# Optimization experiments

Hardware: AMD Instinct MI355X
Metric: run time of the kernel (lower is better)

## Reference

```python
import jax, jax.numpy as jnp
import numpy as np

V, E, H, D = 32000, 512, 512, 3          # vocab, embed_dim, hidden_dim, max_depth
PD = max(H // 4, 16)                      # policy depth-embed dim = 128
DEPTH_EMBED_SCALE = 0.01
SIB_SCALE = 1.0 / np.sqrt(H)              # sibling_scale default 1/sqrt(hidden_dim)
GREEDY_THRESHOLD = 0.5
PROB_MIN, PROB_MAX = 1e-7, 1.0 - 1e-7


def _ln(x, g, b, eps=1e-5):
    m = x.mean(-1, keepdims=True)
    v = jnp.var(x, axis=-1, keepdims=True)
    return (x - m) * jax.lax.rsqrt(v + eps) * g + b


def setup_inputs() -> dict:
    key = jax.random.key(0)
    ks = jax.random.split(key, 12)
    def n(k, shape, s=0.02):
        return jax.random.normal(k, shape, jnp.float32) * s
    return {
        "token_ids": jax.random.randint(ks[0], (4096,), 0, V),
        "emb": n(ks[1], (V, E)),                      # embedding table
        "proj_w": n(ks[2], (H, E), 0.04), "proj_b": jnp.zeros(H, jnp.float32),
        "cf_w": n(ks[3], (2 * H, H), 0.04), "cf_b": jnp.zeros(2 * H, jnp.float32),
        "in_g": jnp.ones(H, jnp.float32), "in_b": jnp.zeros(H, jnp.float32),   # policy input LayerNorm
        "pde": n(ks[4], (D + 1, PD), 0.01),           # policy depth embedding
        "f1w": n(ks[5], (H // 2, H + PD), 0.04), "f1b": jnp.zeros(H // 2, jnp.float32),
        "n1g": jnp.ones(H // 2, jnp.float32), "n1b": jnp.zeros(H // 2, jnp.float32),
        "f2w": n(ks[6], (H // 4, H // 2), 0.06), "f2b": jnp.zeros(H // 4, jnp.float32),
        "n2g": jnp.ones(H // 4, jnp.float32), "n2b": jnp.zeros(H // 4, jnp.float32),
        "pow_w": n(ks[7], (1, H // 4), 0.01), "pow_b": jnp.zeros(1, jnp.float32),
        "sib": n(ks[8], (2, H)),                      # sibling embeddings (left/right)
        "dep": n(ks[9], (D + 1, H), 0.01),            # tree depth embeddings
        "out_w": n(ks[10], (V, H), 0.04), "out_b": jnp.zeros(V, jnp.float32),
    }


def _forward(token_ids, emb, proj_w, proj_b, cf_w, cf_b, in_g, in_b, pde,
             f1w, f1b, n1g, n1b, f2w, f2b, n2g, n2b, pow_w, pow_b,
             sib, dep, out_w, out_b):
    # h0: project token embeddings to hidden space. [N, H]
    h0 = emb[token_ids] @ proj_w.T + proj_b
    nodes = h0[None]                      # level-0 nodes: [1, N, H]
    agg_sum = h0                          # running sum over all tree nodes
    agg_cnt = jnp.float32(1.0)
    alive = jnp.float32(1.0)              # cumulative greedy-expand mask
    for level in range(D):
        # growth policy on the level-mean hidden (+ scaled depth embedding)
        lh = nodes.mean(0) + DEPTH_EMBED_SCALE * dep[level]          # [N, H]
        hn = _ln(lh, in_g, in_b)
        de = jnp.broadcast_to(pde[min(level, D)], (hn.shape[0], PD))
        x = jnp.concatenate([hn, de], axis=-1)
        x = jax.nn.relu(_ln(x @ f1w.T + f1b, n1g, n1b))
        x = jax.nn.relu(_ln(x @ f2w.T + f2b, n2g, n2b))
        p = jax.nn.sigmoid((x @ pow_w.T + pow_b)[..., 0])             # [N]
        p_mean = jnp.clip(p, PROB_MIN, PROB_MAX).mean()
        alive = alive * (p_mean >= GREEDY_THRESHOLD).astype(jnp.float32)
        # binary child expansion: child_fc then chunk into left/right + sibling embeds
        cf = jnp.einsum('mnh,kh->mnk', nodes, cf_w) + cf_b            # [M, N, 2H]
        left = cf[..., :H] + SIB_SCALE * sib[0]
        right = cf[..., H:] + SIB_SCALE * sib[1]
        nodes = jnp.concatenate([left, right], axis=0)                # [2M, N, H]
        agg_sum = agg_sum + alive * nodes.sum(0)
        agg_cnt = agg_cnt + alive * jnp.float32(nodes.shape[0])
    pooled = agg_sum / jnp.maximum(agg_cnt, 1e-8)                     # mean pooling
    return pooled @ out_w.T + out_b                                   # [N, V]


def reference(token_ids, emb, proj_w, proj_b, cf_w, cf_b, in_g, in_b, pde,
              f1w, f1b, n1g, n1b, f2w, f2b, n2g, n2b, pow_w, pow_b,
              sib, dep, out_w, out_b):
    return _forward(token_ids, emb, proj_w, proj_b, cf_w, cf_b, in_g, in_b, pde,
                    f1w, f1b, n1g, n1b, f2w, f2b, n2g, n2b, pow_w, pow_b,
                    sib, dep, out_w, out_b)
```

## Files before the change

### kernel.cpp

```cpp
#include <hip/hip_runtime.h>

typedef unsigned short u16;
using bf16x8 = __attribute__((ext_vector_type(8))) short;
using f32x4  = __attribute__((ext_vector_type(4))) float;

#define SIB_SCALE_F 0.04419417382415922f

__device__ __forceinline__ u16 f2b(float f) {
  unsigned u = __builtin_bit_cast(unsigned, f);
  return (u16)((u + 0x7FFFu + ((u >> 16) & 1u)) >> 16);
}

__device__ __forceinline__ float wred(float v) {
  #pragma unroll
  for (int m = 1; m < 64; m <<= 1) v += __shfl_xor(v, m);
  return v;
}

__device__ __forceinline__ void gload16(const void* g, void* l) {
  __builtin_amdgcn_global_load_lds(
      (const __attribute__((address_space(1))) unsigned int*)g,
      (__attribute__((address_space(3))) unsigned int*)l, 16, 0, 0);
}

__global__ __launch_bounds__(512, 2) void gemmP(
    const u16* __restrict__ A, const u16* __restrict__ B,
    const float* __restrict__ bias,
    float* __restrict__ C, int M, int N, int K, int MT)
{
  __shared__ u16 lds[65536];
  const int t = threadIdx.x, w = t >> 6, lane = t & 63;
  const int wm = w >> 2, wn = w & 3;
  const int r16 = lane & 15, ks = lane >> 4;

  const int bn = blockIdx.y * 256;
  const int mg = blockIdx.x;
  const int NT = K >> 6;
  const int stag = blockIdx.y & (MT - 1);

  auto stageH = [&](const u16* __restrict__ G, int grow0, int kt, int half, int opBase) {
    const int k0 = kt << 6;
    u16* dst = lds + opBase + ((kt & 1) << 14) + (half << 13);
    #pragma unroll
    for (int j = 0; j < 2; ++j) {
      const int r = half * 128 + j * 64 + w * 8 + (lane >> 3);
      const int s = (lane & 7) ^ (r & 7);
      gload16(G + (size_t)(grow0 + r) * K + k0 + s * 8,
              dst + j * 4096 + w * 512);
    }
  };

  for (int mt0 = 0; mt0 < MT; ++mt0) {
    const int mt = (mt0 + stag) & (MT - 1);
    const int bm = (mg * MT + mt) * 256;

    f32x4 acc[8][4];
    #pragma unroll
    for (int m = 0; m < 8; ++m)
      #pragma unroll
      for (int n = 0; n < 4; ++n) {
        f32x4 z = {0.f, 0.f, 0.f, 0.f};
        acc[m][n] = z;
      }

    __builtin_amdgcn_sched_barrier(0);
    stageH(A, bm, 0, 0, 0);
    stageH(A, bm, 0, 1, 0);
    stageH(B, bn, 0, 0, 32768);
    stageH(B, bn, 0, 1, 32768);
    __builtin_amdgcn_sched_barrier(0);
    stageH(B, bn, 1, 0, 32768);
    stageH(B, bn, 1, 1, 32768);
    asm volatile("s_waitcnt vmcnt(4)" ::: "memory");
    __builtin_amdgcn_sched_barrier(0);
    __builtin_amdgcn_s_barrier();

    for (int kt = 0; kt < NT; ++kt) {
      const u16* Ab = lds + ((kt & 1) << 14);
      const u16* Bb = lds + 32768 + ((kt & 1) << 14);
      bf16x8 bfr[4][2];

      #pragma unroll
      for (int p = 0; p < 4; ++p) {
        bf16x8 af2[2][2];
        #pragma unroll
        for (int i = 0; i < 2; ++i) {
          const int row = wm * 128 + (2 * p + i) * 16 + r16;
          af2[i][0] = *(const bf16x8*)(Ab + row * 64 + ((ks ^ (row & 7)) << 3));
          af2[i][1] = *(const bf16x8*)(Ab + row * 64 + (((4 + ks) ^ (row & 7)) << 3));
        }
        if (p == 0) {
          #pragma unroll
          for (int n = 0; n < 4; ++n) {
            const int row = wn * 64 + n * 16 + r16;
            bfr[n][0] = *(const bf16x8*)(Bb + row * 64 + ((ks ^ (row & 7)) << 3));
            bfr[n][1] = *(const bf16x8*)(Bb + row * 64 + (((4 + ks) ^ (row & 7)) << 3));
          }
        }
        if (p == 0 && kt + 1 < NT) stageH(A, bm, kt + 1, 0, 0);
        if (p == 1 && kt + 1 < NT) stageH(A, bm, kt + 1, 1, 0);
        if (p == 2 && kt + 2 < NT) stageH(B, bn, kt + 2, 0, 32768);
        if (p == 3) {
          if (kt + 2 < NT) {
            stageH(B, bn, kt + 2, 1, 32768);
            asm volatile("s_waitcnt vmcnt(4)" ::: "memory");
          } else {
            asm volatile("s_waitcnt vmcnt(0)" ::: "memory");
          }
          __builtin_amdgcn_sched_barrier(0);
        }
        __builtin_amdgcn_s_barrier();
        asm volatile("s_waitcnt lgkmcnt(0)" ::: "memory");
        __builtin_amdgcn_sched_barrier(0);
        __builtin_amdgcn_s_setprio(1);
        #pragma unroll
        for (int i = 0; i < 2; ++i)
          #pragma unroll
          for (int n = 0; n < 4; ++n) {
            acc[2 * p + i][n] = __builtin_amdgcn_mfma_f32_16x16x32_bf16(
                bfr[n][0], af2[i][0], acc[2 * p + i][n], 0, 0, 0);
            acc[2 * p + i][n] = __builtin_amdgcn_mfma_f32_16x16x32_bf16(
                bfr[n][1], af2[i][1], acc[2 * p + i][n], 0, 0, 0);
          }
        __builtin_amdgcn_s_setprio(0);
        __builtin_amdgcn_s_barrier();
      }
    }

    #pragma unroll
    for (int m = 0; m < 8; ++m) {
      const int grow = bm + wm * 128 + m * 16 + r16;
      float* Crow = C + (size_t)grow * N;
      #pragma unroll
      for (int n = 0; n < 4; ++n) {
        const int gcol = bn + wn * 64 + n * 16 + ks * 4;
        const float4 bv = *(const float4*)(bias + gcol);
        f32x4 o;
        o[0] = acc[m][n][0] + bv.x;
        o[1] = acc[m][n][1] + bv.y;
        o[2] = acc[m][n][2] + bv.z;
        o[3] = acc[m][n][3] + bv.w;
        __builtin_nontemporal_store(o, (f32x4*)(Crow + gcol));
      }
    }
  }
}

template <bool GATHER>
__global__ __launch_bounds__(256) void gemm64(
    const float* __restrict__ Afp, const int* __restrict__ tok,
    const u16* __restrict__ A, const u16* __restrict__ B,
    const float* __restrict__ bias, int blvl, float bscale,
    float* __restrict__ C, u16* __restrict__ Cb,
    int M, int N, int K)
{
  __shared__ u16 ldsA[64 * 32];
  __shared__ u16 ldsB[128 * 32];
  const int t = threadIdx.x, w = t >> 6, lane = t & 63;
  const int r16 = lane & 15, ks = lane >> 4;

  const int nb = gridDim.x * gridDim.y;
  const int lid = blockIdx.y * gridDim.x + blockIdx.x;
  const int chunk = nb >> 3;
  const int nlid = (lid & 7) * chunk + (lid >> 3);
  const int bm = (nlid % gridDim.x) * 64;
  const int bn = (nlid / gridDim.x) * 128;

  const int srow = t >> 2, sslot = t & 3;

  f32x4 acc[4][2];
  #pragma unroll
  for (int m = 0; m < 4; ++m)
    #pragma unroll
    for (int n = 0; n < 2; ++n) {
      f32x4 z = {0.f, 0.f, 0.f, 0.f};
      acc[m][n] = z;
    }

  for (int k0 = 0; k0 < K; k0 += 32) {
    if (k0) __syncthreads();
    {
      const int row = srow;
      const int sl = sslot ^ ((row >> 1) & 3);
      if constexpr (GATHER) {
        const float* src = Afp + (size_t)tok[bm + row] * 512 + k0 + sl * 8;
        const float4 a0 = *(const float4*)src;
        const float4 a1 = *(const float4*)(src + 4);
        bf16x8 v;
        v[0] = (short)f2b(a0.x); v[1] = (short)f2b(a0.y);
        v[2] = (short)f2b(a0.z); v[3] = (short)f2b(a0.w);
        v[4] = (short)f2b(a1.x); v[5] = (short)f2b(a1.y);
        v[6] = (short)f2b(a1.z); v[7] = (short)f2b(a1.w);
        *(bf16x8*)(ldsA + t * 8) = v;
      } else {
        gload16(A + (size_t)(bm + row) * K + k0 + sl * 8, ldsA + w * 512);
      }
    }
    #pragma unroll
    for (int i = 0; i < 2; ++i) {
      const int row = i * 64 + srow;
      const int sl = sslot ^ ((row >> 1) & 3);
      gload16(B + (size_t)(bn + row) * K + k0 + sl * 8,
              ldsB + i * 2048 + w * 512);
    }
    __syncthreads();

    bf16x8 af[4], bfr[2];
    #pragma unroll
    for (int m = 0; m < 4; ++m) {
      const int row = m * 16 + r16;
      af[m] = *(const bf16x8*)(ldsA + row * 32 + ((ks ^ ((row >> 1) & 3)) << 3));
    }
    #pragma unroll
    for (int n = 0; n < 2; ++n) {
      const int row = w * 32 + n * 16 + r16;
      bfr[n] = *(const bf16x8*)(ldsB + row * 32 + ((ks ^ ((row >> 1) & 3)) << 3));
    }
    #pragma unroll
    for (int m = 0; m < 4; ++m)
      #pragma unroll
      for (int n = 0; n < 2; ++n)
        acc[m][n] = __builtin_amdgcn_mfma_f32_16x16x32_bf16(bfr[n], af[m], acc[m][n], 0, 0, 0);
  }

  const float* be = bias + (size_t)(bm >> 12) * blvl;
  #pragma unroll
  for (int m = 0; m < 4; ++m) {
    const int grow = bm + m * 16 + r16;
    #pragma unroll
    for (int n = 0; n < 2; ++n) {
      const int gcol = bn + w * 32 + n * 16 + ks * 4;
      const float4 bv = *(const float4*)(be + gcol);
      float4 o;
      o.x = acc[m][n][0] + bv.x * bscale;
      o.y = acc[m][n][1] + bv.y * bscale;
      o.z = acc[m][n][2] + bv.z * bscale;
      o.w = acc[m][n][3] + bv.w * bscale;
      const size_t idx = (size_t)grow * N + gcol;
      *(float4*)(C + idx) = o;
      if (Cb) {
        ushort4 ob = { f2b(o.x), f2b(o.y), f2b(o.z), f2b(o.w) };
        *(ushort4*)(Cb + idx) = ob;
      }
    }
  }
}

__global__ __launch_bounds__(256) void gemm_pool(
    const u16* __restrict__ A, const u16* __restrict__ B,
    const float* __restrict__ bias, float bscale,
    const float* __restrict__ h0f, const float* __restrict__ S1f,
    const float* __restrict__ S2f, const float* __restrict__ psum,
    u16* __restrict__ P,
    int M, int N, int K)
{
  __shared__ u16 ldsA[128 * 32];
  __shared__ u16 ldsB[128 * 32];
  const int t = threadIdx.x;
  const int w = t >> 6;
  const int lane = t & 63;
  const int wr = w >> 1, wc = w & 1;

  const int nb = gridDim.x * gridDim.y;
  const int lid = blockIdx.y * gridDim.x + blockIdx.x;
  const int chunk = nb >> 3;
  const int nlid = (lid & 7) * chunk + (lid >> 3);
  const int bx = nlid % gridDim.x, by = nlid / gridDim.x;

  const int bm = bx * 128, bn = by * 128;
  const int r16 = lane & 15, ks = lane >> 4;
  const int srow = t >> 2, sslot = t & 3;

  f32x4 acc[4][4];
  #pragma unroll
  for (int m = 0; m < 4; ++m)
    #pragma unroll
    for (int n = 0; n < 4; ++n) {
      f32x4 z = {0.f, 0.f, 0.f, 0.f};
      acc[m][n] = z;
    }

  for (int k0 = 0; k0 < K; k0 += 32) {
    if (k0) __syncthreads();
    #pragma unroll
    for (int i = 0; i < 2; ++i) {
      const int row = srow + i * 64;
      const int sl = sslot ^ ((row >> 1) & 3);
      gload16(A + (size_t)(bm + row) * K + k0 + sl * 8,
              ldsA + (i * 2048 + w * 512));
      gload16(B + (size_t)(bn + row) * K + k0 + sl * 8,
              ldsB + (i * 2048 + w * 512));
    }
    __syncthreads();

    bf16x8 af[4], bfr[4];
    #pragma unroll
    for (int m = 0; m < 4; ++m) {
      const int row = wr * 64 + m * 16 + r16;
      af[m] = *(const bf16x8*)(ldsA + row * 32 + ((ks ^ ((row >> 1) & 3)) << 3));
    }
    #pragma unroll
    for (int n = 0; n < 4; ++n) {
      const int row = wc * 64 + n * 16 + r16;
      bfr[n] = *(const bf16x8*)(ldsB + row * 32 + ((ks ^ ((row >> 1) & 3)) << 3));
    }
    #pragma unroll
    for (int m = 0; m < 4; ++m)
      #pragma unroll
      for (int n = 0; n < 4; ++n)
        acc[m][n] = __builtin_amdgcn_mfma_f32_16x16x32_bf16(bfr[n], af[m], acc[m][n], 0, 0, 0);
  }

  const float a0 = (psum[0] * (1.f / 4096.f) >= 0.5f) ? 1.f : 0.f;
  const float a1 = a0 * ((psum[1] * (1.f / 4096.f) >= 0.5f) ? 1.f : 0.f);
  const float a2 = a1 * ((psum[2] * (1.f / 4096.f) >= 0.5f) ? 1.f : 0.f);
  const float cnt = 1.f + a0 * 2.f + a1 * 4.f + a2 * 8.f;
  const float inv = 1.f / fmaxf(cnt, 1e-8f);

  #pragma unroll
  for (int m = 0; m < 4; ++m) {
    const int grow = bm + wr * 64 + m * 16 + r16;
    #pragma unroll
    for (int n = 0; n < 4; ++n) {
      const int gcol = bn + wc * 64 + n * 16 + ks * 4;
      const float4 bv = *(const float4*)(bias + gcol);
      float4 o;
      o.x = acc[m][n][0] + bv.x * bscale;
      o.y = acc[m][n][1] + bv.y * bscale;
      o.z = acc[m][n][2] + bv.z * bscale;
      o.w = acc[m][n][3] + bv.w * bscale;
      const size_t idx = (size_t)grow * N + gcol;
      const float4 h = *(const float4*)(h0f + idx);
      const float4 s1 = *(const float4*)(S1f + idx);
      const float4 s2 = *(const float4*)(S2f + idx);
      ushort4 ob;
      ob.x = f2b((h.x + a0 * s1.x + a1 * s2.x + a2 * o.x) * inv);
      ob.y = f2b((h.y + a0 * s1.y + a1 * s2.y + a2 * o.y) * inv);
      ob.z = f2b((h.z + a0 * s1.z + a1 * s2.z + a2 * o.z) * inv);
      ob.w = f2b((h.w + a0 * s1.w + a1 * s2.w + a2 * o.w) * inv);
      *(ushort4*)(P + idx) = ob;
    }
  }
}

__global__ __launch_bounds__(256) void prep_misc(
    const float* __restrict__ cf_w, const float* __restrict__ cf_b,
    const float* __restrict__ sib, const float* __restrict__ proj_w,
    const float* __restrict__ f1w, const float* __restrict__ f1b,
    const float* __restrict__ f2w, const float* __restrict__ pde,
    const float* __restrict__ out_w,
    u16* __restrict__ wsum_b, u16* __restrict__ projw_b,
    u16* __restrict__ f1w512b, u16* __restrict__ f2wb,
    float* __restrict__ cvec, float* __restrict__ psum,
    float* __restrict__ y1bias, u16* __restrict__ outw_b)
{
  const int b = blockIdx.x, t = threadIdx.x;
  if (b >= 676) {
    const int idx = (b - 676) * 256 + t;
    const float4 v = ((const float4*)out_w)[idx];
    ushort4 o = { f2b(v.x), f2b(v.y), f2b(v.z), f2b(v.w) };
    ((ushort4*)outw_b)[idx] = o;
  } else if (b < 256) {
    const int idx = b * 256 + t;
    const float4 a = ((const float4*)cf_w)[idx];
    const float4 c = ((const float4*)(cf_w + 262144))[idx];
    ushort4 o = { f2b(a.x + c.x), f2b(a.y + c.y), f2b(a.z + c.z), f2b(a.w + c.w) };
    ((ushort4*)wsum_b)[idx] = o;
  } else if (b < 512) {
    const int idx = (b - 256) * 256 + t;
    const float4 v = ((const float4*)proj_w)[idx];
    ushort4 o = { f2b(v.x), f2b(v.y), f2b(v.z), f2b(v.w) };
    ((ushort4*)projw_b)[idx] = o;
  } else if (b < 640) {
    const int fi = (b - 512) * 256 + t;
    const int row = fi >> 7, c4 = fi & 127;
    const float4 v = *(const float4*)(f1w + (size_t)row * 640 + c4 * 4);
    ushort4 o = { f2b(v.x), f2b(v.y), f2b(v.z), f2b(v.w) };
    ((ushort4*)f1w512b)[row * 128 + c4] = o;
  } else if (b < 672) {
    const int idx = (b - 640) * 256 + t;
    const float4 v = ((const float4*)f2w)[idx];
    ushort4 o = { f2b(v.x), f2b(v.y), f2b(v.z), f2b(v.w) };
    ((ushort4*)f2wb)[idx] = o;
  } else if (b < 675) {
    const int l = b - 672, j = t;
    const float* wrow = f1w + (size_t)j * 640 + 512;
    const float* p = pde + l * 128;
    float s = f1b[j];
    #pragma unroll 4
    for (int k = 0; k < 128; ++k) s += wrow[k] * p[k];
    y1bias[l * 256 + j] = s;
  } else {
    cvec[t]       = cf_b[t]       + cf_b[512 + t] + SIB_SCALE_F * (sib[t]       + sib[512 + t]);
    cvec[256 + t] = cf_b[256 + t] + cf_b[768 + t] + SIB_SCALE_F * (sib[256 + t] + sib[768 + t]);
    if (t < 3) psum[t] = 0.f;
  }
}

__global__ __launch_bounds__(256) void mean_ln_concat_b(
    const float* __restrict__ S0, const float* __restrict__ S1,
    const float* __restrict__ S2,
    const float* __restrict__ dep,
    const float* __restrict__ g, const float* __restrict__ b,
    u16* __restrict__ X)
{
  const int wid = threadIdx.x >> 6, lane = threadIdx.x & 63;
  const int gr = blockIdx.x * 4 + wid;
  const int l = gr >> 12, n = gr & 4095;
  const float* Sr = (l == 0 ? S0 : l == 1 ? S1 : S2) + (size_t)n * 512;
  const float invM = (l == 0 ? 1.f : l == 1 ? 0.5f : 0.25f);
  const float* depl = dep + 512 * l;
  const int c0 = lane * 8;
  float x[8];
  float s = 0.f, sq = 0.f;
  #pragma unroll
  for (int i = 0; i < 8; ++i) {
    const float v = Sr[c0 + i] * invM + 0.01f * depl[c0 + i];
    x[i] = v; s += v; sq += v * v;
  }
  s = wred(s); sq = wred(sq);
  const float mean = s * (1.f / 512.f);
  const float var = sq * (1.f / 512.f) - mean * mean;
  const float rs = rsqrtf(var + 1e-5f);
  ushort4 o0, o1;
  o0.x = f2b((x[0] - mean) * rs * g[c0 + 0] + b[c0 + 0]);
  o0.y = f2b((x[1] - mean) * rs * g[c0 + 1] + b[c0 + 1]);
  o0.z = f2b((x[2] - mean) * rs * g[c0 + 2] + b[c0 + 2]);
  o0.w = f2b((x[3] - mean) * rs * g[c0 + 3] + b[c0 + 3]);
  o1.x = f2b((x[4] - mean) * rs * g[c0 + 4] + b[c0 + 4]);
  o1.y = f2b((x[5] - mean) * rs * g[c0 + 5] + b[c0 + 5]);
  o1.z = f2b((x[6] - mean) * rs * g[c0 + 6] + b[c0 + 6]);
  o1.w = f2b((x[7] - mean) * rs * g[c0 + 7] + b[c0 + 7]);
  ushort4* Xr = (ushort4*)(X + (size_t)gr * 512);
  Xr[lane * 2]     = o0;
  Xr[lane * 2 + 1] = o1;
}

__global__ __launch_bounds__(256) void ln_relu_b256(
    const float* __restrict__ X, const float* __restrict__ g,
    const float* __restrict__ b, u16* __restrict__ O)
{
  const int wid = threadIdx.x >> 6, lane = threadIdx.x & 63;
  const int n = blockIdx.x * 4 + wid;
  const float* Xr = X + (size_t)n * 256;
  float x[4];
  float s = 0.f, sq = 0.f;
  #pragma unroll
  for (int i = 0; i < 4; ++i) {
    x[i] = Xr[lane * 4 + i]; s += x[i]; sq += x[i] * x[i];
  }
  s = wred(s); sq = wred(sq);
  const float mean = s * (1.f / 256.f);
  const float var = sq * (1.f / 256.f) - mean * mean;
  const float rs = rsqrtf(var + 1e-5f);
  ushort4 o;
  o.x = f2b(fmaxf((x[0] - mean) * rs * g[lane * 4 + 0] + b[lane * 4 + 0], 0.f));
  o.y = f2b(fmaxf((x[1] - mean) * rs * g[lane * 4 + 1] + b[lane * 4 + 1], 0.f));
  o.z = f2b(fmaxf((x[2] - mean) * rs * g[lane * 4 + 2] + b[lane * 4 + 2], 0.f));
  o.w = f2b(fmaxf((x[3] - mean) * rs * g[lane * 4 + 3] + b[lane * 4 + 3], 0.f));
  ((ushort4*)(O + (size_t)n * 256))[lane] = o;
}

__global__ __launch_bounds__(256) void ln_policy128(
    const float* __restrict__ Y2, const float* __restrict__ g,
    const float* __restrict__ b, const float* __restrict__ pw,
    const float* __restrict__ pb, float* __restrict__ psum)
{
  __shared__ float part[4];
  const int wid = threadIdx.x >> 6, lane = threadIdx.x & 63;
  const int gr = blockIdx.x * 4 + wid;
  const float* Xr = Y2 + (size_t)gr * 128;
  float x[2];
  float s = 0.f, sq = 0.f;
  #pragma unroll
  for (int i = 0; i < 2; ++i) {
    x[i] = Xr[lane * 2 + i]; s += x[i]; sq += x[i] * x[i];
  }
  s = wred(s); sq = wred(sq);
  const float mean = s * (1.f / 128.f);
  const float var = sq * (1.f / 128.f) - mean * mean;
  const float rs = rsqrtf(var + 1e-5f);
  float z = 0.f;
  #pragma unroll
  for (int i = 0; i < 2; ++i) {
    const int c = lane * 2 + i;
    const float v = fmaxf((x[i] - mean) * rs * g[c] + b[c], 0.f);
    z += v * pw[c];
  }
  z = wred(z);
  if (lane == 0) {
    const float p = 1.f / (1.f + expf(-(z + pb[0])));
    part[wid] = fminf(fmaxf(p, 1e-7f), 1.f - 1e-7f);
  }
  __syncthreads();
  if (threadIdx.x == 0)
    atomicAdd(psum + (gr >> 12), part[0] + part[1] + part[2] + part[3]);
}

extern "C" void kernel_launch(void* const* d_in, const int* in_sizes, int n_in,
                              void* d_out, int out_size, void* d_ws, size_t ws_size,
                              hipStream_t stream) {
  const int*   tok    = (const int*)  d_in[0];
  const float* emb    = (const float*)d_in[1];
  const float* proj_w = (const float*)d_in[2];
  const float* proj_b = (const float*)d_in[3];
  const float* cf_w   = (const float*)d_in[4];
  const float* cf_b   = (const float*)d_in[5];
  const float* in_g   = (const float*)d_in[6];
  const float* in_b   = (const float*)d_in[7];
  const float* pde    = (const float*)d_in[8];
  const float* f1w    = (const float*)d_in[9];
  const float* f1b    = (const float*)d_in[10];
  const float* n1g    = (const float*)d_in[11];
  const float* n1b    = (const float*)d_in[12];
  const float* f2w    = (const float*)d_in[13];
  const float* f2bias = (const float*)d_in[14];
  const float* n2g    = (const float*)d_in[15];
  const float* n2b    = (const float*)d_in[16];
  const float* pow_w  = (const float*)d_in[17];
  const float* pow_b  = (const float*)d_in[18];
  const float* sib    = (const float*)d_in[19];
  const float* dep    = (const float*)d_in[20];
  const float* out_w  = (const float*)d_in[21];
  const float* out_b  = (const float*)d_in[22];
  float* out = (float*)d_out;

  char* ws = (char*)d_ws;
  size_t off = 0;
  auto alloc = [&](size_t bytes) -> void* {
    void* p = ws + off;
    off += (bytes + 255) & ~(size_t)255;
    return p;
  };
  u16*   outw_b  = (u16*)  alloc((size_t)32000 * 512 * 2);
  u16*   projw_b = (u16*)  alloc((size_t)512 * 512 * 2);
  u16*   wsum_b  = (u16*)  alloc((size_t)512 * 512 * 2);
  u16*   f1w512b = (u16*)  alloc((size_t)256 * 512 * 2);
  u16*   f2wb    = (u16*)  alloc((size_t)128 * 256 * 2);
  float* h0f     = (float*)alloc((size_t)4096 * 512 * 4);
  u16*   h0b     = (u16*)  alloc((size_t)4096 * 512 * 2);
  float* S1f     = (float*)alloc((size_t)4096 * 512 * 4);
  u16*   S1b     = (u16*)  alloc((size_t)4096 * 512 * 2);
  float* S2f     = (float*)alloc((size_t)4096 * 512 * 4);
  u16*   S2b     = (u16*)  alloc((size_t)4096 * 512 * 2);
  u16*   X       = (u16*)  alloc((size_t)12288 * 512 * 2);
  float* Y1      = (float*)alloc((size_t)12288 * 256 * 4);
  u16*   Y1b     = (u16*)  alloc((size_t)12288 * 256 * 2);
  float* Y2      = (float*)alloc((size_t)12288 * 128 * 4);
  float* y1bias  = (float*)alloc(3 * 256 * 4);
  float* cvec    = (float*)alloc(512 * 4);
  float* psum    = (float*)alloc(256);
  u16*   poolb   = (u16*)  alloc((size_t)4096 * 512 * 2);

  prep_misc<<<16676, 256, 0, stream>>>(cf_w, cf_b, sib, proj_w, f1w, f1b, f2w,
                                       pde, out_w,
                                       wsum_b, projw_b, f1w512b, f2wb,
                                       cvec, psum, y1bias, outw_b);

  gemm64<true><<<dim3(64, 4), 256, 0, stream>>>(
      emb, tok, nullptr, projw_b, proj_b, 0, 1.f, h0f, h0b, 4096, 512, 512);
  gemm64<false><<<dim3(64, 4), 256, 0, stream>>>(
      nullptr, nullptr, h0b, wsum_b, cvec, 0, 1.f, S1f, S1b, 4096, 512, 512);
  gemm64<false><<<dim3(64, 4), 256, 0, stream>>>(
      nullptr, nullptr, S1b, wsum_b, cvec, 0, 2.f, S2f, S2b, 4096, 512, 512);

  mean_ln_concat_b<<<3072, 256, 0, stream>>>(h0f, S1f, S2f, dep, in_g, in_b, X);
  gemm64<false><<<dim3(192, 2), 256, 0, stream>>>(
      nullptr, nullptr, X, f1w512b, y1bias, 256, 1.f, Y1, nullptr, 12288, 256, 512);
  ln_relu_b256<<<3072, 256, 0, stream>>>(Y1, n1g, n1b, Y1b);
  gemm64<false><<<dim3(192, 1), 256, 0, stream>>>(
      nullptr, nullptr, Y1b, f2wb, f2bias, 0, 1.f, Y2, nullptr, 12288, 128, 256);
  ln_policy128<<<3072, 256, 0, stream>>>(Y2, n2g, n2b, pow_w, pow_b, psum);

  gemm_pool<<<dim3(32, 4), 256, 0, stream>>>(
      S2b, wsum_b, cvec, 4.f, h0f, S1f, S2f, psum, poolb, 4096, 512, 512);

  gemmP<<<dim3(2, 125), 512, 0, stream>>>(poolb, outw_b, out_b,
                                          out, 4096, 32000, 512, 8);
}
```

Measured before the change: 380.1 us.

## Shrink output GEMM tiles and overlap epilogue stores with next tile's mainloop

New measurement: 467.8 us. +23.1%, slower.

```diff
diff --git a/kernel.cpp b/kernel.cpp
--- a/kernel.cpp
+++ b/kernel.cpp
@@ -23,71 +23,73 @@
       (__attribute__((address_space(3))) unsigned int*)l, 16, 0, 0);
 }
 
-__global__ __launch_bounds__(512, 2) void gemmP(
+__global__ __launch_bounds__(256, 2) void gemmT(
     const u16* __restrict__ A, const u16* __restrict__ B,
     const float* __restrict__ bias,
     float* __restrict__ C, int M, int N, int K, int MT)
 {
-  __shared__ u16 lds[65536];
+  __shared__ u16 lds[32768];
   const int t = threadIdx.x, w = t >> 6, lane = t & 63;
-  const int wm = w >> 2, wn = w & 3;
+  const int wm = w >> 1, wn = w & 1;
   const int r16 = lane & 15, ks = lane >> 4;
-
-  const int bn = blockIdx.y * 256;
+  const int bn = blockIdx.y * 128;
   const int mg = blockIdx.x;
-  const int NT = K >> 6;
   const int stag = blockIdx.y & (MT - 1);
 
-  auto stageH = [&](const u16* __restrict__ G, int grow0, int kt, int half, int opBase) {
-    const int k0 = kt << 6;
-    u16* dst = lds + opBase + ((kt & 1) << 14) + (half << 13);
-    #pragma unroll
-    for (int j = 0; j < 2; ++j) {
-      const int r = half * 128 + j * 64 + w * 8 + (lane >> 3);
+  auto stageT = [&](const u16* __restrict__ G, int grow0, int ktile, int buf, int base) {
+    const int k0 = ktile << 6;
+    u16* dst = lds + base + (buf << 13);
+    #pragma unroll
+    for (int j = 0; j < 4; ++j) {
+      const int r = j * 32 + w * 8 + (lane >> 3);
       const int s = (lane & 7) ^ (r & 7);
       gload16(G + (size_t)(grow0 + r) * K + k0 + s * 8,
-              dst + j * 4096 + w * 512);
+              dst + j * 2048 + w * 512);
     }
   };
 
-  for (int mt0 = 0; mt0 < MT; ++mt0) {
-    const int mt = (mt0 + stag) & (MT - 1);
-    const int bm = (mg * MT + mt) * 256;
-
-    f32x4 acc[8][4];
-    #pragma unroll
-    for (int m = 0; m < 8; ++m)
-      #pragma unroll
-      for (int n = 0; n < 4; ++n) {
-        f32x4 z = {0.f, 0.f, 0.f, 0.f};
-        acc[m][n] = z;
-      }
-
-    __builtin_amdgcn_sched_barrier(0);
-    stageH(A, bm, 0, 0, 0);
-    stageH(A, bm, 0, 1, 0);
-    stageH(B, bn, 0, 0, 32768);
-    stageH(B, bn, 0, 1, 32768);
-    __builtin_amdgcn_sched_barrier(0);
-    stageH(B, bn, 1, 0, 32768);
-    stageH(B, bn, 1, 1, 32768);
+  float4 biasv[4];
+  #pragma unroll
+  for (int n = 0; n < 4; ++n)
+    biasv[n] = *(const float4*)(bias + bn + wn * 64 + n * 16 + ks * 4);
+
+  f32x4 acc[4][4], pacc[4][4];
+  #pragma unroll
+  for (int m = 0; m < 4; ++m)
+    #pragma unroll
+    for (int n = 0; n < 4; ++n) {
+      f32x4 z = {0.f, 0.f, 0.f, 0.f};
+      acc[m][n] = z; pacc[m][n] = z;
+    }
+  int bmPrev = 0;
+
+  {
+    const int bm0 = (mg * MT + (stag & (MT - 1))) * 128;
+    stageT(A, bm0, 0, 0, 0);
+    stageT(B, bn, 0, 0, 16384);
+    stageT(B, bn, 1, 1, 16384);
     asm volatile("s_waitcnt vmcnt(4)" ::: "memory");
     __builtin_amdgcn_sched_barrier(0);
     __builtin_amdgcn_s_barrier();
-
-    for (int kt = 0; kt < NT; ++kt) {
-      const u16* Ab = lds + ((kt & 1) << 14);
-      const u16* Bb = lds + 32768 + ((kt & 1) << 14);
+  }
+
+  for (int mt = 0; mt < MT; ++mt) {
+    const int bm = (mg * MT + ((mt + stag) & (MT - 1))) * 128;
+    const int bmNext = (mg * MT + ((mt + 1 + stag) & (MT - 1))) * 128;
+
+    #pragma unroll
+    for (int kt = 0; kt < 8; ++kt) {
+      const u16* Ab = lds + ((kt & 1) << 13);
+      const u16* Bb = lds + 16384 + ((kt & 1) << 13);
       bf16x8 bfr[4][2];
 
       #pragma unroll
       for (int p = 0; p < 4; ++p) {
-        bf16x8 af2[2][2];
-        #pragma unroll
-        for (int i = 0; i < 2; ++i) {
-          const int row = wm * 128 + (2 * p + i) * 16 + r16;
-          af2[i][0] = *(const bf16x8*)(Ab + row * 64 + ((ks ^ (row & 7)) << 3));
-          af2[i][1] = *(const bf16x8*)(Ab + row * 64 + (((4 + ks) ^ (row & 7)) << 3));
+        bf16x8 af[2];
+        {
+          const int row = wm * 64 + p * 16 + r16;
+          af[0] = *(const bf16x8*)(Ab + row * 64 + ((ks ^ (row & 7)) << 3));
+          af[1] = *(const bf16x8*)(Ab + row * 64 + (((4 + ks) ^ (row & 7)) << 3));
         }
         if (p == 0) {
           #pragma unroll
@@ -96,16 +98,41 @@
             bfr[n][0] = *(const bf16x8*)(Bb + row * 64 + ((ks ^ (row & 7)) << 3));
             bfr[n][1] = *(const bf16x8*)(Bb + row * 64 + (((4 + ks) ^ (row & 7)) << 3));
           }
+          if (kt < 7)             stageT(A, bm,     kt + 1, (kt + 1) & 1, 0);
+          else if (mt < MT - 1)   stageT(A, bmNext, 0,      0,            0);
         }
-        if (p == 0 && kt + 1 < NT) stageH(A, bm, kt + 1, 0, 0);
-        if (p == 1 && kt + 1 < NT) stageH(A, bm, kt + 1, 1, 0);
-        if (p == 2 && kt + 2 < NT) stageH(B, bn, kt + 2, 0, 32768);
+        if (p == 1 && kt == 0 && mt > 0) {
+          #pragma unroll
+          for (int m = 0; m < 4; ++m) {
+            const int grow = bmPrev + wm * 64 + m * 16 + r16;
+            float* Crow = C + (size_t)grow * N;
+            #pragma unroll
+            for (int n = 0; n < 4; ++n) {
+              const int gcol = bn + wn * 64 + n * 16 + ks * 4;
+              f32x4 o;
+              o[0] = pacc[m][n][0] + biasv[n].x;
+              o[1] = pacc[m][n][1] + biasv[n].y;
+              o[2] = pacc[m][n][2] + biasv[n].z;
+              o[3] = pacc[m][n][3] + biasv[n].w;
+              __builtin_nontemporal_store(o, (f32x4*)(Crow + gcol));
+            }
+          }
+        }
+        if (p == 2) {
+          if (kt < 6)             stageT(B, bn, kt + 2,       kt & 1, 16384);
+          else if (mt < MT - 1)   stageT(B, bn, (kt + 2) & 7, kt & 1, 16384);
+        }
         if (p == 3) {
-          if (kt + 2 < NT) {
-            stageH(B, bn, kt + 2, 1, 32768);
+          if (kt == 0) {
+            if (mt > 0) { asm volatile("s_waitcnt vmcnt(20)" ::: "memory"); }
+            else        { asm volatile("s_waitcnt vmcnt(4)"  ::: "memory"); }
+          } else if (kt < 6) {
             asm volatile("s_waitcnt vmcnt(4)" ::: "memory");
+          } else if (kt == 6) {
+            if (mt < MT - 1) { asm volatile("s_waitcnt vmcnt(4)" ::: "memory"); }
+            else             { asm volatile("s_waitcnt vmcnt(0)" ::: "memory"); }
           } else {
-            asm volatile("s_waitcnt vmcnt(0)" ::: "memory");
+            if (mt < MT - 1) { asm volatile("s_waitcnt vmcnt(4)" ::: "memory"); }
           }
           __builtin_amdgcn_sched_barrier(0);
         }
@@ -114,34 +141,39 @@
         __builtin_amdgcn_sched_barrier(0);
         __builtin_amdgcn_s_setprio(1);
         #pragma unroll
-        for (int i = 0; i < 2; ++i)
-          #pragma unroll
-          for (int n = 0; n < 4; ++n) {
-            acc[2 * p + i][n] = __builtin_amdgcn_mfma_f32_16x16x32_bf16(
-                bfr[n][0], af2[i][0], acc[2 * p + i][n], 0, 0, 0);
-            acc[2 * p + i][n] = __builtin_amdgcn_mfma_f32_16x16x32_bf16(
-                bfr[n][1], af2[i][1], acc[2 * p + i][n], 0, 0, 0);
-          }
+        for (int n = 0; n < 4; ++n) {
+          acc[p][n] = __builtin_amdgcn_mfma_f32_16x16x32_bf16(bfr[n][0], af[0], acc[p][n], 0, 0, 0);
+          acc[p][n] = __builtin_amdgcn_mfma_f32_16x16x32_bf16(bfr[n][1], af[1], acc[p][n], 0, 0, 0);
+        }
         __builtin_amdgcn_s_setprio(0);
         __builtin_amdgcn_s_barrier();
       }
     }
 
-    #pragma unroll
-    for (int m = 0; m < 8; ++m) {
-      const int grow = bm + wm * 128 + m * 16 + r16;
-      float* Crow = C + (size_t)grow * N;
+    bmPrev = bm;
+    #pragma unroll
+    for (int m = 0; m < 4; ++m)
       #pragma unroll
       for (int n = 0; n < 4; ++n) {
-        const int gcol = bn + wn * 64 + n * 16 + ks * 4;
-        const float4 bv = *(const float4*)(bias + gcol);
-        f32x4 o;
-        o[0] = acc[m][n][0] + bv.x;
-        o[1] = acc[m][n][1] + bv.y;
-        o[2] = acc[m][n][2] + bv.z;
-        o[3] = acc[m][n][3] + bv.w;
-        __builtin_nontemporal_store(o, (f32x4*)(Crow + gcol));
+        pacc[m][n] = acc[m][n];
+        f32x4 z = {0.f, 0.f, 0.f, 0.f};
+        acc[m][n] = z;
       }
+  }
+
+  #pragma unroll
+  for (int m = 0; m < 4; ++m) {
+    const int grow = bmPrev + wm * 64 + m * 16 + r16;
+    float* Crow = C + (size_t)grow * N;
+    #pragma unroll
+    for (int n = 0; n < 4; ++n) {
+      const int gcol = bn + wn * 64 + n * 16 + ks * 4;
+      f32x4 o;
+      o[0] = pacc[m][n][0] + biasv[n].x;
+      o[1] = pacc[m][n][1] + biasv[n].y;
+      o[2] = pacc[m][n][2] + biasv[n].z;
+      o[3] = pacc[m][n][3] + biasv[n].w;
+      __builtin_nontemporal_store(o, (f32x4*)(Crow + gcol));
     }
   }
 }
@@ -575,6 +607,6 @@
   gemm_pool<<<dim3(32, 4), 256, 0, stream>>>(
       S2b, wsum_b, cvec, 4.f, h0f, S1f, S2f, psum, poolb, 4096, 512, 512);
 
-  gemmP<<<dim3(2, 125), 512, 0, stream>>>(poolb, outw_b, out_b,
-                                          out, 4096, 32000, 512, 8);
-}
+  gemmT<<<dim3(2, 250), 256, 0, stream>>>(poolb, outw_b, out_b,
+                                          out, 4096, 32000, 512, 16);
+}
```
